# Performance work log

Measured on AMD Instinct MI355X. Metric: run time of the kernel, lower is better.

Reference implementation:

```python
import jax, jax.numpy as jnp
import numpy as np

B, IN, OUT = 131072, 512, 512


def setup_inputs() -> dict:
    key = jax.random.key(0)
    k1, k2 = jax.random.split(key)
    x = jax.random.normal(k1, (B, IN), dtype=jnp.float32)
    # matches reset_parameters: normal(0, sqrt(1/in_features))
    weight = jax.random.normal(k2, (OUT, IN), dtype=jnp.float32) * jnp.sqrt(1.0 / IN)
    bias = jnp.zeros((OUT,), dtype=jnp.float32)
    return {"x": x, "weight": weight, "bias": bias}


def _binarize(w):
    # deterministic sign binarization: w >= 0 -> +1, else -1
    return jnp.where(w >= 0, 1.0, -1.0).astype(w.dtype)


def reference(x, weight, bias):
    wb = _binarize(weight)            # [out, in], values in {-1, +1}
    # out = x @ wb.T + bias           # [B, out]
    return jnp.einsum("bi,oi->bo", x, wb) + bias
```

## Files before the change

### kernel.cpp

```cpp
#include <hip/hip_runtime.h>
#include <stdint.h>


#define BATCH   131072
#define IN_F    512
#define OUT_F   512
#define BM      64
#define NCH     8
#define BUFB    16384

using f32x4  = __attribute__((ext_vector_type(4))) float;
using f32x16 = __attribute__((ext_vector_type(16))) float;
using short8 = __attribute__((ext_vector_type(8))) short;
using usv8   = __attribute__((ext_vector_type(8))) unsigned short;
using u32    = uint32_t;

__global__ void prep_w(const float* __restrict__ W, unsigned short* __restrict__ wf) {
    int t = blockIdx.x * blockDim.x + threadIdx.x;
    int l  = t & 63;
    int nf = (t >> 6) & 15;
    int kt = t >> 10;
    int n = nf * 32 + (l & 31);
    int k = kt * 16 + ((l >> 5) << 3);
    const float* src = W + (size_t)n * IN_F + k;
    f32x4 w0 = *(const f32x4*)(src);
    f32x4 w1 = *(const f32x4*)(src + 4);
    usv8 o;
#pragma unroll
    for (int j = 0; j < 4; ++j) {
        o[j]     = (w0[j] >= 0.0f) ? 0x3F80u : 0xBF80u;
        o[j + 4] = (w1[j] >= 0.0f) ? 0x3F80u : 0xBF80u;
    }
    *(usv8*)(wf + (size_t)t * 8) = o;
}

__device__ __forceinline__ void wait_vm6() { asm volatile("s_waitcnt vmcnt(6)" ::: "memory"); }
__device__ __forceinline__ void wait_vm4() { asm volatile("s_waitcnt vmcnt(4)" ::: "memory"); }

__global__ __launch_bounds__(512, 4) void gemm_bin(
    const float* __restrict__ X, const unsigned short* __restrict__ WF,
    const float* __restrict__ bias, float* __restrict__ out) {

    __shared__ __align__(16) char smem[4 * BUFB];

    const int tid  = threadIdx.x;
    const int lane = tid & 63;
    const int wv   = tid >> 6;
    const int m0   = blockIdx.x * BM;

    const int dr   = wv * 4 + (lane >> 4);
    const int dc   = (lane & 15) * 16;
    const int dswz = (dr & 7) << 4;
    const float* src0 = X + (size_t)(m0 + dr) * IN_F + ((dc ^ dswz) >> 2);
    const float* src1 = src0 + (size_t)32 * IN_F;

#define ISSUE_DMA(ck_)                                                         \
    {                                                                          \
        char* b_ = smem + ((ck_) & 3) * BUFB + wv * 1024;                      \
        __builtin_amdgcn_global_load_lds(                                      \
            (const __attribute__((address_space(1))) void*)(src0 + (ck_) * 64),\
            (__attribute__((address_space(3))) void*)(b_), 16, 0, 0);          \
        __builtin_amdgcn_global_load_lds(                                      \
            (const __attribute__((address_space(1))) void*)(src1 + (ck_) * 64),\
            (__attribute__((address_space(3))) void*)(b_ + 8192), 16, 0, 0);   \
    }

    const short8* wb = (const short8*)(WF) + ((size_t)(wv * 2) * 64 + lane);
#define LDB(dst, g_)                                                           \
    {                                                                          \
        _Pragma("unroll")                                                      \
        for (int fn = 0; fn < 2; ++fn)                                         \
            dst[fn] = wb[(g_) * 1024 + fn * 64];                               \
    }

    const int arow = (lane & 31) * 256;
    const int aq32 = (lane >> 5) << 5;
    const int aswz = (lane & 7) << 4;

#define LDA_CVT(dst, ab_, kt4_)                                                \
    {                                                                          \
        _Pragma("unroll")                                                      \
        for (int rg = 0; rg < 2; ++rg) {                                       \
            const char* p_  = (ab_) + rg * 8192 + arow;                        \
            const int  blo_ = (((kt4_) << 6) + aq32) ^ aswz;                   \
            f32x4 lo_ = *(const f32x4*)(p_ + blo_);                            \
            f32x4 hi_ = *(const f32x4*)(p_ + (blo_ ^ 16));                     \
            u32 w0_, w1_, w2_, w3_;                                            \
            asm("v_cvt_pk_bf16_f32 %0, %1, %2" : "=v"(w0_)                     \
                : "v"(lo_[0]), "v"(lo_[1]));                                   \
            asm("v_cvt_pk_bf16_f32 %0, %1, %2" : "=v"(w1_)                     \
                : "v"(lo_[2]), "v"(lo_[3]));                                   \
            asm("v_cvt_pk_bf16_f32 %0, %1, %2" : "=v"(w2_)                     \
                : "v"(hi_[0]), "v"(hi_[1]));                                   \
            asm("v_cvt_pk_bf16_f32 %0, %1, %2" : "=v"(w3_)                     \
                : "v"(hi_[2]), "v"(hi_[3]));                                   \
            union { u32 w[4]; short8 v; } pk_;                                 \
            pk_.w[0] = w0_; pk_.w[1] = w1_; pk_.w[2] = w2_; pk_.w[3] = w3_;    \
            dst[rg] = pk_.v;                                                   \
        }                                                                      \
    }

    f32x16 acc[2][2];
#pragma unroll
    for (int fn = 0; fn < 2; ++fn) {
        const float bv = bias[wv * 64 + fn * 32 + (lane & 31)];
#pragma unroll
        for (int rg = 0; rg < 2; ++rg)
#pragma unroll
            for (int r = 0; r < 16; ++r) acc[rg][fn][r] = bv;
    }

    ISSUE_DMA(0);
    ISSUE_DMA(1);

    short8 bf[2][2];
#pragma unroll
    for (int ck = 0; ck < NCH; ++ck) {
        LDB(bf[0], ck * 4 + 0);
        LDB(bf[1], ck * 4 + 1);
        __builtin_amdgcn_sched_barrier(0);
        if (ck < NCH - 1) wait_vm6(); else wait_vm4();
        __builtin_amdgcn_sched_barrier(0);
        __builtin_amdgcn_s_barrier();
        __builtin_amdgcn_sched_barrier(0);
        if (ck + 2 < NCH) ISSUE_DMA(ck + 2);

        const char* ab = smem + (ck & 3) * BUFB;
        short8 af[2];
#pragma unroll
        for (int kt4 = 0; kt4 < 4; ++kt4) {
            LDA_CVT(af, ab, kt4);
#pragma unroll
            for (int rg = 0; rg < 2; ++rg)
#pragma unroll
                for (int fn = 0; fn < 2; ++fn)
                    acc[rg][fn] = __builtin_amdgcn_mfma_f32_32x32x16_bf16(
                        af[rg], bf[kt4 & 1][fn], acc[rg][fn], 0, 0, 0);
            if (kt4 < 2) LDB(bf[kt4 & 1], ck * 4 + kt4 + 2);
        }
    }
#undef ISSUE_DMA
#undef LDB
#undef LDA_CVT

    const int c     = lane & 31;
    const int rbase = (lane >> 5) << 2;
#pragma unroll
    for (int rg = 0; rg < 2; ++rg)
#pragma unroll
        for (int fn = 0; fn < 2; ++fn)
#pragma unroll
            for (int r = 0; r < 16; ++r) {
                const int row = rg * 32 + (r & 3) + 8 * (r >> 2) + rbase;
                out[(size_t)(m0 + row) * OUT_F + wv * 64 + fn * 32 + c] =
                    acc[rg][fn][r];
            }
}

extern "C" void kernel_launch(void* const* d_in, const int* in_sizes, int n_in,
                              void* d_out, int out_size, void* d_ws, size_t ws_size,
                              hipStream_t stream) {
    const float* X    = (const float*)d_in[0];
    const float* W    = (const float*)d_in[1];
    const float* bias = (const float*)d_in[2];
    float* o          = (float*)d_out;
    unsigned short* wf = (unsigned short*)d_ws;

    hipLaunchKernelGGL(prep_w, dim3(128), dim3(256), 0, stream, W, wf);
    hipLaunchKernelGGL(gemm_bin, dim3(BATCH / BM), dim3(512), 0, stream,
                       X, wf, bias, o);
}
```

Baseline: 136.7 us.

## Prefetch whole B chunk a step ahead, widen LDS swizzle, add MFMA priority

Loads all B fragments for the next K chunk a full iteration early into a double-buffered register array, replacing the per-kt4 refill, and retunes the vmcnt waits to match. It also widens the XOR swizzle from 8 to 16 lanes so LDS reads conflict less, and raises wave priority around the MFMA groups. Launch bounds drop from 4 to 2 blocks per CU so the extra B registers fit. The aim is to hide global B load latency and LDS bank conflicts, at the cost of higher register use and lower occupancy.

```diff
diff --git a/kernel.cpp b/kernel.cpp
--- a/kernel.cpp
+++ b/kernel.cpp
@@ -34,10 +34,7 @@
     *(usv8*)(wf + (size_t)t * 8) = o;
 }
 
-__device__ __forceinline__ void wait_vm6() { asm volatile("s_waitcnt vmcnt(6)" ::: "memory"); }
-__device__ __forceinline__ void wait_vm4() { asm volatile("s_waitcnt vmcnt(4)" ::: "memory"); }
-
-__global__ __launch_bounds__(512, 4) void gemm_bin(
+__global__ __launch_bounds__(512, 2) void gemm_bin(
     const float* __restrict__ X, const unsigned short* __restrict__ WF,
     const float* __restrict__ bias, float* __restrict__ out) {
 
@@ -49,9 +46,8 @@
     const int m0   = blockIdx.x * BM;
 
     const int dr   = wv * 4 + (lane >> 4);
-    const int dc   = (lane & 15) * 16;
-    const int dswz = (dr & 7) << 4;
-    const float* src0 = X + (size_t)(m0 + dr) * IN_F + ((dc ^ dswz) >> 2);
+    const int ds4  = ((lane & 15) ^ (dr & 15)) << 2;
+    const float* src0 = X + (size_t)(m0 + dr) * IN_F + ds4;
     const float* src1 = src0 + (size_t)32 * IN_F;
 
 #define ISSUE_DMA(ck_)                                                         \
@@ -66,16 +62,19 @@
     }
 
     const short8* wb = (const short8*)(WF) + ((size_t)(wv * 2) * 64 + lane);
-#define LDB(dst, g_)                                                           \
+    short8 bf[2][4][2];
+#define LDB_ALL(bi_, ck_)                                                      \
     {                                                                          \
         _Pragma("unroll")                                                      \
-        for (int fn = 0; fn < 2; ++fn)                                         \
-            dst[fn] = wb[(g_) * 1024 + fn * 64];                               \
+        for (int g = 0; g < 4; ++g)                                            \
+            _Pragma("unroll")                                                  \
+            for (int fn = 0; fn < 2; ++fn)                                     \
+                bf[bi_][g][fn] = wb[((ck_) * 4 + g) * 1024 + fn * 64];         \
     }
 
     const int arow = (lane & 31) * 256;
     const int aq32 = (lane >> 5) << 5;
-    const int aswz = (lane & 7) << 4;
+    const int aswz = (lane & 15) << 4;
 
 #define LDA_CVT(dst, ab_, kt4_)                                                \
     {                                                                          \
@@ -109,38 +108,44 @@
 #pragma unroll
             for (int r = 0; r < 16; ++r) acc[rg][fn][r] = bv;
     }
+    __builtin_amdgcn_sched_barrier(0);
 
     ISSUE_DMA(0);
+    __builtin_amdgcn_sched_barrier(0);
+    LDB_ALL(0, 0);
+    __builtin_amdgcn_sched_barrier(0);
     ISSUE_DMA(1);
+    __builtin_amdgcn_sched_barrier(0);
 
-    short8 bf[2][2];
 #pragma unroll
     for (int ck = 0; ck < NCH; ++ck) {
-        LDB(bf[0], ck * 4 + 0);
-        LDB(bf[1], ck * 4 + 1);
+        if (ck + 1 < NCH) LDB_ALL((ck + 1) & 1, ck + 1);
         __builtin_amdgcn_sched_barrier(0);
-        if (ck < NCH - 1) wait_vm6(); else wait_vm4();
+        if (ck < NCH - 1) asm volatile("s_waitcnt vmcnt(18)" ::: "memory");
+        else              asm volatile("s_waitcnt vmcnt(8)"  ::: "memory");
         __builtin_amdgcn_sched_barrier(0);
         __builtin_amdgcn_s_barrier();
         __builtin_amdgcn_sched_barrier(0);
         if (ck + 2 < NCH) ISSUE_DMA(ck + 2);
+        __builtin_amdgcn_sched_barrier(0);
 
         const char* ab = smem + (ck & 3) * BUFB;
         short8 af[2];
 #pragma unroll
         for (int kt4 = 0; kt4 < 4; ++kt4) {
             LDA_CVT(af, ab, kt4);
+            __builtin_amdgcn_s_setprio(1);
 #pragma unroll
             for (int rg = 0; rg < 2; ++rg)
 #pragma unroll
                 for (int fn = 0; fn < 2; ++fn)
                     acc[rg][fn] = __builtin_amdgcn_mfma_f32_32x32x16_bf16(
-                        af[rg], bf[kt4 & 1][fn], acc[rg][fn], 0, 0, 0);
-            if (kt4 < 2) LDB(bf[kt4 & 1], ck * 4 + kt4 + 2);
+                        af[rg], bf[ck & 1][kt4][fn], acc[rg][fn], 0, 0, 0);
+            __builtin_amdgcn_s_setprio(0);
         }
     }
 #undef ISSUE_DMA
-#undef LDB
+#undef LDB_ALL
 #undef LDA_CVT
 
     const int c     = lane & 31;
```

Measured after the change: 141.8 us. +3.7%, slower.
